# Kernel optimization log

Hardware: AMD Instinct MI355X
Metric: run time of the kernel (lower is better)

Reference implementation:

```python
import jax, jax.numpy as jnp
import numpy as np

N = 100000        # nodes
E = 1600000       # edges (avg degree 16)
IN = 128          # in_channels
HID = 256         # hidden_channels
OUT = 2           # out_channels
G = 512           # num graphs in batch


def setup_inputs() -> dict:
    key = jax.random.key(0)
    ks = jax.random.split(key, 10)
    x = jax.random.normal(ks[0], (N, IN), dtype=jnp.float32)
    edge_index = jax.random.randint(ks[1], (2, E), 0, N, dtype=jnp.int64)
    # sorted graph assignment, every graph non-empty (PyG-style batching)
    batch = (jnp.arange(N, dtype=jnp.int64) * G) // N
    s = 1.0 / np.sqrt(IN)
    sh = 1.0 / np.sqrt(2 * HID)
    sh1 = 1.0 / np.sqrt(HID)
    W_l = jax.random.uniform(ks[2], (HID, IN), jnp.float32, -s, s)   # SAGE lin_l (neighbors)
    b_l = jax.random.uniform(ks[3], (HID,), jnp.float32, -s, s)
    W_r = jax.random.uniform(ks[4], (HID, IN), jnp.float32, -s, s)   # SAGE lin_r (root), no bias
    W0 = jax.random.uniform(ks[5], (HID, IN), jnp.float32, -s, s)    # lin0
    b0 = jax.random.uniform(ks[5], (HID,), jnp.float32, -s, s)
    W1 = jax.random.uniform(ks[6], (HID, 2 * HID), jnp.float32, -sh, sh)  # lin1
    b1 = jax.random.uniform(ks[7], (HID,), jnp.float32, -sh, sh)
    W2 = jax.random.uniform(ks[8], (OUT, HID), jnp.float32, -sh1, sh1)    # lin2
    b2 = jax.random.uniform(ks[9], (OUT,), jnp.float32, -sh1, sh1)
    return {"x": x, "edge_index": edge_index, "batch": batch,
            "W_l": W_l, "b_l": b_l, "W_r": W_r,
            "W0": W0, "b0": b0, "W1": W1, "b1": b1, "W2": W2, "b2": b2}


def reference(x, edge_index, batch, W_l, b_l, W_r, W0, b0, W1, b1, W2, b2):
    src, dst = edge_index[0], edge_index[1]
    # SAGEConv: mean-aggregate neighbor features (gather -> scatter-add -> normalize)
    msg_sum = jax.ops.segment_sum(x[src], dst, num_segments=N)          # [N, IN]
    deg = jax.ops.segment_sum(jnp.ones((E,), x.dtype), dst, num_segments=N)
    aggr = msg_sum / jnp.maximum(deg, 1.0)[:, None]
    h = jax.nn.relu(aggr @ W_l.T + b_l + x @ W_r.T)                     # [N, HID]
    # global max pool per graph
    hp = jax.ops.segment_max(h, batch, num_segments=G)                  # [G, HID]
    # root node = first node of each graph (batch is sorted)
    root = jnp.searchsorted(batch, jnp.arange(G, dtype=batch.dtype))    # [G]
    news = jax.nn.relu(x[root] @ W0.T + b0)                             # [G, HID]
    h = jax.nn.relu(jnp.concatenate([news, hp], axis=-1) @ W1.T + b1)   # [G, HID]
    h = h @ W2.T + b2                                                   # [G, OUT]
    return jax.nn.log_softmax(h, axis=-1)
```

## Files before the change

kernel.cpp:

```cpp
#include <hip/hip_runtime.h>
#include <hip/hip_bf16.h>
#include <math.h>
#include <stdint.h>

#define IN_C 128
#define HID  256
#define OUT_C 2

#define BSHIFT 9
#define BNODES 512
#define EPB 4096

typedef __attribute__((ext_vector_type(8))) short short8;
typedef __attribute__((ext_vector_type(4))) float f32x4;
typedef __attribute__((ext_vector_type(2))) float f32x2;

#if defined(__has_builtin)
#if __has_builtin(__builtin_amdgcn_cvt_pk_f32_fp8) && __has_builtin(__builtin_amdgcn_cvt_pk_fp8_f32)
#define HAVE_FP8_CVT 1
#endif
#if __has_builtin(__builtin_amdgcn_global_load_lds)
#define HAVE_GLL 1
#endif
#endif

__device__ __forceinline__ ushort f2bf(float f) {
  uint32_t u = __float_as_uint(f);
  uint32_t r = u + 0x7FFF + ((u >> 16) & 1);
  return (ushort)(r >> 16);
}
__device__ __forceinline__ float bf2f(ushort b) {
  return __uint_as_float(((uint32_t)b) << 16);
}

#ifndef HAVE_FP8_CVT
__device__ __forceinline__ uint32_t f2fp8_1(float f) {
  uint32_t u = __float_as_uint(f);
  uint32_t s = (u >> 24) & 0x80;
  float a = fabsf(f);
  if (a >= 448.f) return s | 0x7E;
  if (a < 0.015625f) {
    uint32_t m = (uint32_t)(a * 512.f + 0.5f);
    return s | m;
  }
  uint32_t r = u & 0x7fffffff;
  r += 0x7FFFF + ((r >> 20) & 1);
  uint32_t e = (r >> 23) - 127;
  if ((int)e > 8) return s | 0x7E;
  return s | ((e + 7) << 3) | ((r >> 20) & 7);
}
__device__ __forceinline__ float fp8_2f(uint32_t b) {
  uint32_t s = (b & 0x80) << 24;
  uint32_t e = (b >> 3) & 0xF, m = b & 7;
  if (e == 0) { float f = (float)m * 0.001953125f; return s ? -f : f; }
  return __uint_as_float(s | ((e + 120) << 23) | (m << 20));
}
#endif

__device__ __forceinline__ void acc8f8(float* s, uint2 v) {
#ifdef HAVE_FP8_CVT
  f32x2 a = __builtin_amdgcn_cvt_pk_f32_fp8(v.x, false);
  f32x2 b = __builtin_amdgcn_cvt_pk_f32_fp8(v.x, true);
  f32x2 c = __builtin_amdgcn_cvt_pk_f32_fp8(v.y, false);
  f32x2 d = __builtin_amdgcn_cvt_pk_f32_fp8(v.y, true);
  s[0] += a.x; s[1] += a.y; s[2] += b.x; s[3] += b.y;
  s[4] += c.x; s[5] += c.y; s[6] += d.x; s[7] += d.y;
#else
  s[0] += fp8_2f(v.x & 0xff);        s[1] += fp8_2f((v.x >> 8) & 0xff);
  s[2] += fp8_2f((v.x >> 16) & 0xff); s[3] += fp8_2f(v.x >> 24);
  s[4] += fp8_2f(v.y & 0xff);        s[5] += fp8_2f((v.y >> 8) & 0xff);
  s[6] += fp8_2f((v.y >> 16) & 0xff); s[7] += fp8_2f(v.y >> 24);
#endif
}


__global__ void k_hist(const int* __restrict__ dst, int* __restrict__ bcount, int E) {
  __shared__ int h[256];
  int t = threadIdx.x;
  h[t] = 0;
  __syncthreads();
  for (int e = blockIdx.x * 256 + t; e < E; e += gridDim.x * 256)
    atomicAdd(&h[dst[e] >> BSHIFT], 1);
  __syncthreads();
  if (h[t]) atomicAdd(&bcount[t], h[t]);
}

__global__ void k_bucket_scan(const int* __restrict__ bcount,
                              int* __restrict__ bbase, int* __restrict__ bcursor) {
  __shared__ int sd[256];
  int t = threadIdx.x;
  int cnt = bcount[t];
  sd[t] = cnt;
  __syncthreads();
  for (int off = 1; off < 256; off <<= 1) {
    int v = (t >= off) ? sd[t - off] : 0;
    __syncthreads();
    sd[t] += v;
    __syncthreads();
  }
  int base = sd[t] - cnt;
  bbase[t] = base;
  bcursor[t] = base;
}

__global__ __launch_bounds__(256) void k_scatter(
    const int* __restrict__ src, const int* __restrict__ dst,
    int* __restrict__ bcursor, uint32_t* __restrict__ rec, int E) {
  __shared__ int h[256];
  __shared__ int bbase[256];
  __shared__ int lcur[256];
  int t = threadIdx.x;
  int e0 = blockIdx.x * EPB;
  int e1 = e0 + EPB < E ? e0 + EPB : E;
  h[t] = 0; lcur[t] = 0;
  __syncthreads();
  for (int e = e0 + t; e < e1; e += 256)
    atomicAdd(&h[dst[e] >> BSHIFT], 1);
  __syncthreads();
  if (h[t]) bbase[t] = atomicAdd(&bcursor[t], h[t]);
  __syncthreads();
  for (int e = e0 + t; e < e1; e += 256) {
    int d = dst[e];
    int b = d >> BSHIFT;
    int r = atomicAdd(&lcur[b], 1);
    rec[bbase[b] + r] = ((uint32_t)src[e] << BSHIFT) | ((uint32_t)d & (BNODES - 1));
  }
}

__global__ __launch_bounds__(256) void k_csr(
    const uint32_t* __restrict__ rec, const int* __restrict__ bbase,
    const int* __restrict__ bcount,
    int* __restrict__ row_start, int* __restrict__ deg,
    int* __restrict__ csr, int n) {
  __shared__ int ldeg[BNODES];
  __shared__ int lexcl[BNODES];
  __shared__ int ssum[256];
  int t = threadIdx.x;
  int b = blockIdx.x;
  int node0 = b << BSHIFT;
  int ebase = bbase[b];
  int ecnt = bcount[b];

  ldeg[t] = 0; ldeg[t + 256] = 0;
  __syncthreads();
  for (int i = t; i < ecnt; i += 256)
    atomicAdd(&ldeg[rec[ebase + i] & (BNODES - 1)], 1);
  __syncthreads();

  int v0 = ldeg[2 * t], v1 = ldeg[2 * t + 1];
  ssum[t] = v0 + v1;
  __syncthreads();
  for (int off = 1; off < 256; off <<= 1) {
    int v = (t >= off) ? ssum[t - off] : 0;
    __syncthreads();
    ssum[t] += v;
    __syncthreads();
  }
  int excl = ssum[t] - (v0 + v1);
  lexcl[2 * t] = excl;
  lexcl[2 * t + 1] = excl + v0;
  int node = node0 + 2 * t;
  if (node < n) { row_start[node] = ebase + excl; deg[node] = v0; }
  if (node + 1 < n) { row_start[node + 1] = ebase + excl + v0; deg[node + 1] = v1; }
  ldeg[2 * t] = 0; ldeg[2 * t + 1] = 0;
  __syncthreads();
  for (int i = t; i < ecnt; i += 256) {
    uint32_t r = rec[ebase + i];
    int li = r & (BNODES - 1);
    int k = atomicAdd(&ldeg[li], 1);
    csr[ebase + lexcl[li] + k] = (int)(r >> BSHIFT);
  }
}


__global__ void k_cast(const float* __restrict__ in, ushort* __restrict__ outb,
                       uint32_t* __restrict__ outf8, int n4) {
  int i = blockIdx.x * 256 + threadIdx.x;
  if (i < n4) {
    float4 v = ((const float4*)in)[i];
    ushort4 o;
    o.x = f2bf(v.x); o.y = f2bf(v.y); o.z = f2bf(v.z); o.w = f2bf(v.w);
    ((ushort4*)outb)[i] = o;
#ifdef HAVE_FP8_CVT
    int p = __builtin_amdgcn_cvt_pk_fp8_f32(v.x, v.y, 0, false);
    p = __builtin_amdgcn_cvt_pk_fp8_f32(v.z, v.w, p, true);
    outf8[i] = (uint32_t)p;
#else
    outf8[i] = f2fp8_1(v.x) | (f2fp8_1(v.y) << 8) | (f2fp8_1(v.z) << 16) |
               (f2fp8_1(v.w) << 24);
#endif
  }
}

__global__ void k_wcat(const float* __restrict__ Wl, const float* __restrict__ Wr,
                       ushort* __restrict__ Wcat) {
  int c = blockIdx.x, k = threadIdx.x;
  float v = (k < IN_C) ? Wl[(size_t)c * IN_C + k] : Wr[(size_t)c * IN_C + (k - IN_C)];
  Wcat[(size_t)c * (2 * IN_C) + k] = f2bf(v);
}


__global__ void k_aggr(const uint32_t* __restrict__ xf8, const int* __restrict__ csr,
                       const int* __restrict__ row_start, const int* __restrict__ deg,
                       ushort* __restrict__ aggr, int n) {
  int wid = threadIdx.x >> 6;
  int lane = threadIdx.x & 63;
  int node = blockIdx.x * 4 + wid;
  if (node >= n) return;
  int base = row_start[node];
  int d = deg[node];
  int q = lane >> 4, li = lane & 15;
  float s[8] = {};
  int i = q;
  for (; i + 12 < d; i += 16) {
    int n0 = csr[base + i];
    int n1 = csr[base + i + 4];
    int n2 = csr[base + i + 8];
    int n3 = csr[base + i + 12];
    uint2 a = ((const uint2*)(xf8 + (size_t)n0 * (IN_C / 4)))[li];
    uint2 b = ((const uint2*)(xf8 + (size_t)n1 * (IN_C / 4)))[li];
    uint2 c = ((const uint2*)(xf8 + (size_t)n2 * (IN_C / 4)))[li];
    uint2 e = ((const uint2*)(xf8 + (size_t)n3 * (IN_C / 4)))[li];
    acc8f8(s, a); acc8f8(s, b); acc8f8(s, c); acc8f8(s, e);
  }
  for (; i < d; i += 4) {
    int n0 = csr[base + i];
    uint2 a = ((const uint2*)(xf8 + (size_t)n0 * (IN_C / 4)))[li];
    acc8f8(s, a);
  }
#pragma unroll
  for (int j = 0; j < 8; ++j) {
    s[j] += __shfl_xor(s[j], 16);
    s[j] += __shfl_xor(s[j], 32);
  }
  if (q == 0) {
    float inv = 1.0f / (float)(d > 1 ? d : 1);
    uint4 o;
    o.x = (uint32_t)f2bf(s[0] * inv) | ((uint32_t)f2bf(s[1] * inv) << 16);
    o.y = (uint32_t)f2bf(s[2] * inv) | ((uint32_t)f2bf(s[3] * inv) << 16);
    o.z = (uint32_t)f2bf(s[4] * inv) | ((uint32_t)f2bf(s[5] * inv) << 16);
    o.w = (uint32_t)f2bf(s[6] * inv) | ((uint32_t)f2bf(s[7] * inv) << 16);
    ((uint4*)(aggr + (size_t)node * IN_C))[li] = o;
  }
}


#ifdef HAVE_GLL
__device__ __forceinline__ void load16_lds(const ushort* g, ushort* l) {
  __builtin_amdgcn_global_load_lds(
      (const __attribute__((address_space(1))) uint32_t*)g,
      (__attribute__((address_space(3))) uint32_t*)l, 16, 0, 0);
}
#endif

__global__ __launch_bounds__(256) void k_gemm_pool(
    const ushort* __restrict__ aggrb, const ushort* __restrict__ xb,
    const ushort* __restrict__ Wcat, const float* __restrict__ bl,
    const int* __restrict__ batch, float* __restrict__ hp, int n) {
  __shared__ ushort sA[2][64 * 32];
  __shared__ ushort sB[2][256 * 32];
  __shared__ float sbl[256];
  __shared__ int sBatch[64];

  int t = threadIdx.x;
  int n0 = blockIdx.x * 64;
  sbl[t] = bl[t];
  if (t < 64) sBatch[t] = (n0 + t < n) ? batch[n0 + t] : -1;

  int lane = t & 63, w = t >> 6;
  int q = lane >> 4, m = lane & 15;

  int rA = t >> 2, pA = t & 3;
  int cA = pA ^ ((rA >> 1) & 3);
  int gnA = n0 + rA; gnA = gnA < n ? gnA : n - 1;
  const ushort* baseAggr = aggrb + (size_t)gnA * IN_C + cA * 8;
  const ushort* baseX    = xb + (size_t)gnA * IN_C + cA * 8;
  int ldsA = rA * 32 + pA * 8;
  int pchunk = q ^ ((m >> 1) & 3);

  f32x4 acc[4][4] = {};

#ifdef HAVE_GLL
  auto stage = [&](int k0, int buf) {
    const ushort* srcA = (k0 < 4) ? baseAggr + k0 * 32 : baseX + (k0 - 4) * 32;
    load16_lds(srcA, &sA[buf][ldsA]);
#pragma unroll
    for (int it = 0; it < 4; ++it) {
      int rB = it * 64 + (t >> 2);
      int cB = (t & 3) ^ ((rB >> 1) & 3);
      load16_lds(Wcat + (size_t)rB * (2 * IN_C) + k0 * 32 + cB * 8,
                 &sB[buf][rB * 32 + (t & 3) * 8]);
    }
  };
  stage(0, 0);
  __syncthreads();
#pragma unroll
  for (int k0 = 0; k0 < 8; ++k0) {
    int cur = k0 & 1;
    if (k0 < 7) stage(k0 + 1, cur ^ 1);
    short8 af[4], bf[4];
#pragma unroll
    for (int rt = 0; rt < 4; ++rt)
      af[rt] = *(const short8*)&sA[cur][(rt * 16 + m) * 32 + pchunk * 8];
#pragma unroll
    for (int ct = 0; ct < 4; ++ct)
      bf[ct] = *(const short8*)&sB[cur][(w * 64 + ct * 16 + m) * 32 + pchunk * 8];
#pragma unroll
    for (int rt = 0; rt < 4; ++rt)
#pragma unroll
      for (int ct = 0; ct < 4; ++ct)
        acc[rt][ct] = __builtin_amdgcn_mfma_f32_16x16x32_bf16(af[rt], bf[ct], acc[rt][ct], 0, 0, 0);
    __syncthreads();
  }
#else
  for (int k0 = 0; k0 < 8; ++k0) {
    const ushort* srcA = (k0 < 4) ? baseAggr + k0 * 32 : baseX + (k0 - 4) * 32;
    uint4 vA = *(const uint4*)srcA;
    uint4 vB[4];
#pragma unroll
    for (int it = 0; it < 4; ++it) {
      int rB = it * 64 + (t >> 2);
      int cB = (t & 3) ^ ((rB >> 1) & 3);
      vB[it] = *(const uint4*)(Wcat + (size_t)rB * (2 * IN_C) + k0 * 32 + cB * 8);
    }
    __syncthreads();
    *(uint4*)&sA[0][ldsA] = vA;
#pragma unroll
    for (int it = 0; it < 4; ++it) {
      int rB = it * 64 + (t >> 2);
      *(uint4*)&sB[0][rB * 32 + (t & 3) * 8] = vB[it];
    }
    __syncthreads();
    short8 af[4], bf[4];
#pragma unroll
    for (int rt = 0; rt < 4; ++rt)
      af[rt] = *(const short8*)&sA[0][(rt * 16 + m) * 32 + pchunk * 8];
#pragma unroll
    for (int ct = 0; ct < 4; ++ct)
      bf[ct] = *(const short8*)&sB[0][(w * 64 + ct * 16 + m) * 32 + pchunk * 8];
#pragma unroll
    for (int rt = 0; rt < 4; ++rt)
#pragma unroll
      for (int ct = 0; ct < 4; ++ct)
        acc[rt][ct] = __builtin_amdgcn_mfma_f32_16x16x32_bf16(af[rt], bf[ct], acc[rt][ct], 0, 0, 0);
  }
#endif

  int last = n - 1 - n0; last = last < 63 ? last : 63;
  int gA = sBatch[0];
  int gB = sBatch[last];
#pragma unroll
  for (int ct = 0; ct < 4; ++ct) {
    int col = w * 64 + ct * 16 + m;
    float bias = sbl[col];
    float mA = 0.f, mB = 0.f;
#pragma unroll
    for (int rt = 0; rt < 4; ++rt) {
#pragma unroll
      for (int i = 0; i < 4; ++i) {
        int lr = rt * 16 + q * 4 + i;
        if (n0 + lr < n) {
          float v = fmaxf(acc[rt][ct][i] + bias, 0.f);
          if (sBatch[lr] == gA) mA = fmaxf(mA, v);
          else mB = fmaxf(mB, v);
        }
      }
    }
    mA = fmaxf(mA, __shfl_xor(mA, 16)); mA = fmaxf(mA, __shfl_xor(mA, 32));
    mB = fmaxf(mB, __shfl_xor(mB, 16)); mB = fmaxf(mB, __shfl_xor(mB, 32));
    if (q == 0) {
      atomicMax((int*)&hp[(size_t)gA * HID + col], __float_as_int(mA));
      if (gB != gA) atomicMax((int*)&hp[(size_t)gB * HID + col], __float_as_int(mB));
    }
  }
}


__global__ void k_root(const int* __restrict__ batch, int* __restrict__ root, int n) {
  int i = blockIdx.x * 256 + threadIdx.x;
  if (i < n) {
    int g = batch[i];
    if (i == 0 || batch[i - 1] != g) root[g] = i;
  }
}


__global__ __launch_bounds__(256) void k_mlp2(
    const float* __restrict__ x, const float* __restrict__ hp,
    const int* __restrict__ root,
    const float* __restrict__ W0, const float* __restrict__ b0,
    const float* __restrict__ W1, const float* __restrict__ b1,
    const float* __restrict__ W2, const float* __restrict__ b2,
    float* __restrict__ out) {
  __shared__ float xr[IN_C];
  __shared__ float cat[2 * HID];
  __shared__ float h2r[HID];
  __shared__ float red[8];

  int g = blockIdx.x;
  int t = threadIdx.x;
  int rg = root[g];
  if (t < IN_C) xr[t] = x[(size_t)rg * IN_C + t];
  __syncthreads();

  float a0 = b0[t];
  const float* w0 = W0 + (size_t)t * IN_C;
#pragma unroll 4
  for (int k = 0; k < IN_C; ++k) a0 += xr[k] * w0[k];
  cat[t] = fmaxf(a0, 0.f);
  cat[HID + t] = hp[(size_t)g * HID + t];
  __syncthreads();

  float a1 = b1[t];
  const float* w1 = W1 + (size_t)t * (2 * HID);
#pragma unroll 4
  for (int j = 0; j < 2 * HID; ++j) a1 += cat[j] * w1[j];
  h2r[t] = fmaxf(a1, 0.f);
  __syncthreads();

  float p0 = h2r[t] * W2[t];
  float p1 = h2r[t] * W2[HID + t];
  for (int off = 32; off > 0; off >>= 1) {
    p0 += __shfl_down(p0, off);
    p1 += __shfl_down(p1, off);
  }
  int lane = t & 63, wid = t >> 6;
  if (lane == 0) { red[wid * 2] = p0; red[wid * 2 + 1] = p1; }
  __syncthreads();
  if (t == 0) {
    float l0 = b2[0] + red[0] + red[2] + red[4] + red[6];
    float l1 = b2[1] + red[1] + red[3] + red[5] + red[7];
    float mx = fmaxf(l0, l1);
    float ls = logf(expf(l0 - mx) + expf(l1 - mx));
    out[(size_t)g * 2 + 0] = l0 - mx - ls;
    out[(size_t)g * 2 + 1] = l1 - mx - ls;
  }
}


extern "C" void kernel_launch(void* const* d_in, const int* in_sizes, int n_in,
                              void* d_out, int out_size, void* d_ws, size_t ws_size,
                              hipStream_t stream) {
  const float* x  = (const float*)d_in[0];
  const int* ei   = (const int*)d_in[1];
  const int* batch= (const int*)d_in[2];
  const float* Wl = (const float*)d_in[3];
  const float* bl = (const float*)d_in[4];
  const float* Wr = (const float*)d_in[5];
  const float* W0 = (const float*)d_in[6];
  const float* b0 = (const float*)d_in[7];
  const float* W1 = (const float*)d_in[8];
  const float* b1 = (const float*)d_in[9];
  const float* W2 = (const float*)d_in[10];
  const float* b2 = (const float*)d_in[11];
  float* out = (float*)d_out;

  const int N = in_sizes[0] / IN_C;
  const int E = in_sizes[1] / 2;
  const int G = out_size / OUT_C;
  const int* src = ei;
  const int* dst = ei + E;
  const int NB = (N + BNODES - 1) >> BSHIFT;

  char* w = (char*)d_ws;
  int* deg       = (int*)w; w += (size_t)N * 4;
  int* row_start = (int*)w; w += (size_t)N * 4;
  int* bcount    = (int*)w; w += 1024;
  int* bbase     = (int*)w; w += 1024;
  int* bcursor   = (int*)w; w += 1024;
  int* root      = (int*)w; w += (size_t)G * 4;
  w = (char*)(((uintptr_t)w + 255) & ~(uintptr_t)255);
  int* csr       = (int*)w; w += (size_t)E * 4;
  w = (char*)(((uintptr_t)w + 255) & ~(uintptr_t)255);
  ushort* xb     = (ushort*)w; w += (size_t)N * IN_C * 2;
  uint32_t* xf8  = (uint32_t*)w; w += (size_t)N * IN_C;
  ushort* aggrb  = (ushort*)w; w += (size_t)N * IN_C * 2;
  ushort* Wcat   = (ushort*)w; w += (size_t)HID * (2 * IN_C) * 2;
  float* hp      = (float*)w; w += (size_t)G * HID * 4;
  uint32_t* rec  = (uint32_t*)aggrb;

  hipMemsetAsync(bcount, 0, 1024, stream);
  hipMemsetAsync(hp, 0, (size_t)G * HID * 4, stream);

  k_cast<<<((N * IN_C / 4) + 255) / 256, 256, 0, stream>>>(x, xb, xf8, N * IN_C / 4);
  k_wcat<<<HID, 2 * IN_C, 0, stream>>>(Wl, Wr, Wcat);
  k_hist<<<1024, 256, 0, stream>>>(dst, bcount, E);
  k_bucket_scan<<<1, 256, 0, stream>>>(bcount, bbase, bcursor);
  k_scatter<<<(E + EPB - 1) / EPB, 256, 0, stream>>>(src, dst, bcursor, rec, E);
  k_csr<<<NB, 256, 0, stream>>>(rec, bbase, bcount, row_start, deg, csr, N);
  k_root<<<(N + 255) / 256, 256, 0, stream>>>(batch, root, N);
  k_aggr<<<(N + 3) / 4, 256, 0, stream>>>(xf8, csr, row_start, deg, aggrb, N);
  k_gemm_pool<<<(N + 63) / 64, 256, 0, stream>>>(aggrb, xb, Wcat, bl, batch, hp, N);
  k_mlp2<<<G, 256, 0, stream>>>(x, hp, root, W0, b0, W1, b1, W2, b2, out);
}
```

Measured before the change: 331.3 us.

## Batch MLP head over 64 graphs per block using bf16 MFMA

```diff
diff --git a/kernel.cpp b/kernel.cpp
--- a/kernel.cpp
+++ b/kernel.cpp
@@ -197,6 +197,23 @@
   int c = blockIdx.x, k = threadIdx.x;
   float v = (k < IN_C) ? Wl[(size_t)c * IN_C + k] : Wr[(size_t)c * IN_C + (k - IN_C)];
   Wcat[(size_t)c * (2 * IN_C) + k] = f2bf(v);
+}
+
+__global__ void k_cast2(const float* __restrict__ W0, const float* __restrict__ W1,
+                        ushort* __restrict__ W0b, ushort* __restrict__ W1b) {
+  const int N0 = HID * IN_C / 4;
+  const int N1 = HID * 2 * HID / 4;
+  int i = blockIdx.x * 256 + threadIdx.x;
+  if (i < N0) {
+    float4 v = ((const float4*)W0)[i];
+    ushort4 o = {f2bf(v.x), f2bf(v.y), f2bf(v.z), f2bf(v.w)};
+    ((ushort4*)W0b)[i] = o;
+  } else if (i < N0 + N1) {
+    int j = i - N0;
+    float4 v = ((const float4*)W1)[j];
+    ushort4 o = {f2bf(v.x), f2bf(v.y), f2bf(v.z), f2bf(v.w)};
+    ((ushort4*)W1b)[j] = o;
+  }
 }
 
 
@@ -385,55 +402,145 @@
 }
 
 
-__global__ __launch_bounds__(256) void k_mlp2(
-    const float* __restrict__ x, const float* __restrict__ hp,
+__global__ __launch_bounds__(256) void k_tail(
+    const ushort* __restrict__ xb, const float* __restrict__ hp,
     const int* __restrict__ root,
-    const float* __restrict__ W0, const float* __restrict__ b0,
-    const float* __restrict__ W1, const float* __restrict__ b1,
+    const ushort* __restrict__ W0b, const float* __restrict__ b0,
+    const ushort* __restrict__ W1b, const float* __restrict__ b1,
     const float* __restrict__ W2, const float* __restrict__ b2,
-    float* __restrict__ out) {
-  __shared__ float xr[IN_C];
-  __shared__ float cat[2 * HID];
-  __shared__ float h2r[HID];
-  __shared__ float red[8];
-
-  int g = blockIdx.x;
+    float* __restrict__ out, int G) {
+  __shared__ ushort sCat[64][264];
+  __shared__ int sRoot[64];
+  __shared__ float pp[256][2];
+
   int t = threadIdx.x;
-  int rg = root[g];
-  if (t < IN_C) xr[t] = x[(size_t)rg * IN_C + t];
-  __syncthreads();
-
-  float a0 = b0[t];
-  const float* w0 = W0 + (size_t)t * IN_C;
-#pragma unroll 4
-  for (int k = 0; k < IN_C; ++k) a0 += xr[k] * w0[k];
-  cat[t] = fmaxf(a0, 0.f);
-  cat[HID + t] = hp[(size_t)g * HID + t];
-  __syncthreads();
-
-  float a1 = b1[t];
-  const float* w1 = W1 + (size_t)t * (2 * HID);
-#pragma unroll 4
-  for (int j = 0; j < 2 * HID; ++j) a1 += cat[j] * w1[j];
-  h2r[t] = fmaxf(a1, 0.f);
-  __syncthreads();
-
-  float p0 = h2r[t] * W2[t];
-  float p1 = h2r[t] * W2[HID + t];
-  for (int off = 32; off > 0; off >>= 1) {
-    p0 += __shfl_down(p0, off);
-    p1 += __shfl_down(p1, off);
-  }
-  int lane = t & 63, wid = t >> 6;
-  if (lane == 0) { red[wid * 2] = p0; red[wid * 2 + 1] = p1; }
-  __syncthreads();
-  if (t == 0) {
-    float l0 = b2[0] + red[0] + red[2] + red[4] + red[6];
-    float l1 = b2[1] + red[1] + red[3] + red[5] + red[7];
+  int g0 = blockIdx.x * 64;
+  if (t < 64) sRoot[t] = (g0 + t < G) ? root[g0 + t] : 0;
+  __syncthreads();
+
+  int lane = t & 63, w = t >> 6;
+  int q = lane >> 4, m = lane & 15;
+
+  const ushort* xrow[4];
+#pragma unroll
+  for (int rt = 0; rt < 4; ++rt)
+    xrow[rt] = xb + (size_t)sRoot[rt * 16 + m] * IN_C;
+
+  {
+    f32x4 acc[4][4] = {};
+#pragma unroll
+    for (int kc = 0; kc < 4; ++kc) {
+      short8 af[4], bf[4];
+#pragma unroll
+      for (int rt = 0; rt < 4; ++rt)
+        af[rt] = *(const short8*)(xrow[rt] + kc * 32 + q * 8);
+#pragma unroll
+      for (int ct = 0; ct < 4; ++ct) {
+        int col = w * 64 + ct * 16 + m;
+        bf[ct] = *(const short8*)(W0b + (size_t)col * IN_C + kc * 32 + q * 8);
+      }
+#pragma unroll
+      for (int rt = 0; rt < 4; ++rt)
+#pragma unroll
+        for (int ct = 0; ct < 4; ++ct)
+          acc[rt][ct] = __builtin_amdgcn_mfma_f32_16x16x32_bf16(af[rt], bf[ct], acc[rt][ct], 0, 0, 0);
+    }
+#pragma unroll
+    for (int ct = 0; ct < 4; ++ct) {
+      int col = w * 64 + ct * 16 + m;
+      float bias = b0[col];
+#pragma unroll
+      for (int rt = 0; rt < 4; ++rt)
+#pragma unroll
+        for (int i = 0; i < 4; ++i) {
+          int row = rt * 16 + q * 4 + i;
+          sCat[row][col] = f2bf(fmaxf(acc[rt][ct][i] + bias, 0.f));
+        }
+    }
+  }
+  __syncthreads();
+
+  f32x4 acc2[4][4] = {};
+#pragma unroll
+  for (int kc = 0; kc < 8; ++kc) {
+    short8 af[4], bf[4];
+#pragma unroll
+    for (int rt = 0; rt < 4; ++rt)
+      af[rt] = *(const short8*)&sCat[rt * 16 + m][kc * 32 + q * 8];
+#pragma unroll
+    for (int ct = 0; ct < 4; ++ct) {
+      int col = w * 64 + ct * 16 + m;
+      bf[ct] = *(const short8*)(W1b + (size_t)col * (2 * HID) + kc * 32 + q * 8);
+    }
+#pragma unroll
+    for (int rt = 0; rt < 4; ++rt)
+#pragma unroll
+      for (int ct = 0; ct < 4; ++ct)
+        acc2[rt][ct] = __builtin_amdgcn_mfma_f32_16x16x32_bf16(af[rt], bf[ct], acc2[rt][ct], 0, 0, 0);
+  }
+  __syncthreads();
+#pragma unroll
+  for (int it = 0; it < 16; ++it) {
+    int idx = it * 256 + t;
+    int r = idx >> 6, c4 = (idx & 63) * 4;
+    if (g0 + r < G) {
+      float4 v = *(const float4*)(hp + (size_t)(g0 + r) * HID + c4);
+      ushort4 o = {f2bf(v.x), f2bf(v.y), f2bf(v.z), f2bf(v.w)};
+      *(ushort4*)&sCat[r][c4] = o;
+    }
+  }
+  __syncthreads();
+#pragma unroll
+  for (int kc = 8; kc < 16; ++kc) {
+    short8 af[4], bf[4];
+#pragma unroll
+    for (int rt = 0; rt < 4; ++rt)
+      af[rt] = *(const short8*)&sCat[rt * 16 + m][(kc - 8) * 32 + q * 8];
+#pragma unroll
+    for (int ct = 0; ct < 4; ++ct) {
+      int col = w * 64 + ct * 16 + m;
+      bf[ct] = *(const short8*)(W1b + (size_t)col * (2 * HID) + kc * 32 + q * 8);
+    }
+#pragma unroll
+    for (int rt = 0; rt < 4; ++rt)
+#pragma unroll
+      for (int ct = 0; ct < 4; ++ct)
+        acc2[rt][ct] = __builtin_amdgcn_mfma_f32_16x16x32_bf16(af[rt], bf[ct], acc2[rt][ct], 0, 0, 0);
+  }
+  __syncthreads();
+#pragma unroll
+  for (int ct = 0; ct < 4; ++ct) {
+    int col = w * 64 + ct * 16 + m;
+    float bias = b1[col];
+#pragma unroll
+    for (int rt = 0; rt < 4; ++rt)
+#pragma unroll
+      for (int i = 0; i < 4; ++i) {
+        int row = rt * 16 + q * 4 + i;
+        sCat[row][col] = f2bf(fmaxf(acc2[rt][ct][i] + bias, 0.f));
+      }
+  }
+  __syncthreads();
+
+  {
+    int row = t >> 2, qq = t & 3;
+    float p0 = 0.f, p1 = 0.f;
+    for (int c = qq * 64; c < qq * 64 + 64; ++c) {
+      float hv = bf2f(sCat[row][c]);
+      p0 += hv * W2[c];
+      p1 += hv * W2[HID + c];
+    }
+    pp[t][0] = p0; pp[t][1] = p1;
+  }
+  __syncthreads();
+  if (t < 64 && g0 + t < G) {
+    float l0 = b2[0], l1 = b2[1];
+#pragma unroll
+    for (int k = 0; k < 4; ++k) { l0 += pp[t * 4 + k][0]; l1 += pp[t * 4 + k][1]; }
     float mx = fmaxf(l0, l1);
     float ls = logf(expf(l0 - mx) + expf(l1 - mx));
-    out[(size_t)g * 2 + 0] = l0 - mx - ls;
-    out[(size_t)g * 2 + 1] = l1 - mx - ls;
+    out[(size_t)(g0 + t) * 2 + 0] = l0 - mx - ls;
+    out[(size_t)(g0 + t) * 2 + 1] = l1 - mx - ls;
   }
 }
 
@@ -476,6 +583,8 @@
   uint32_t* xf8  = (uint32_t*)w; w += (size_t)N * IN_C;
   ushort* aggrb  = (ushort*)w; w += (size_t)N * IN_C * 2;
   ushort* Wcat   = (ushort*)w; w += (size_t)HID * (2 * IN_C) * 2;
+  ushort* W0b    = (ushort*)w; w += (size_t)HID * IN_C * 2;
+  ushort* W1b    = (ushort*)w; w += (size_t)HID * 2 * HID * 2;
   float* hp      = (float*)w; w += (size_t)G * HID * 4;
   uint32_t* rec  = (uint32_t*)aggrb;
 
@@ -484,6 +593,7 @@
 
   k_cast<<<((N * IN_C / 4) + 255) / 256, 256, 0, stream>>>(x, xb, xf8, N * IN_C / 4);
   k_wcat<<<HID, 2 * IN_C, 0, stream>>>(Wl, Wr, Wcat);
+  k_cast2<<<(HID * IN_C / 4 + HID * 2 * HID / 4 + 255) / 256, 256, 0, stream>>>(W0, W1, W0b, W1b);
   k_hist<<<1024, 256, 0, stream>>>(dst, bcount, E);
   k_bucket_scan<<<1, 256, 0, stream>>>(bcount, bbase, bcursor);
   k_scatter<<<(E + EPB - 1) / EPB, 256, 0, stream>>>(src, dst, bcursor, rec, E);
@@ -491,5 +601,5 @@
   k_root<<<(N + 255) / 256, 256, 0, stream>>>(batch, root, N);
   k_aggr<<<(N + 3) / 4, 256, 0, stream>>>(xf8, csr, row_start, deg, aggrb, N);
   k_gemm_pool<<<(N + 63) / 64, 256, 0, stream>>>(aggrb, xb, Wcat, bl, batch, hp, N);
-  k_mlp2<<<G, 256, 0, stream>>>(x, hp, root, W0, b0, W1, b1, W2, b2, out);
-}
+  k_tail<<<(G + 63) / 64, 256, 0, stream>>>(xb, hp, root, W0b, b0, W1b, b1, W2, b2, out, G);
+}
```

Measured after the change: 302.2 us. -8.8%, faster.
